# Optimization experiments

Measured on AMD Instinct MI355X. Metric: run time of the kernel, lower is better.

## Reference

```python
import jax, jax.numpy as jnp
import numpy as np

LOG2 = float(np.log(2.0))

def ssp(x):
    # shifted softplus, the PhysNet-family activation: softplus(x) - ln(2)
    return jax.nn.softplus(x) - LOG2

def setup_inputs() -> dict:
    key = jax.random.key(0)
    k1, k2, k3, k4, k5 = jax.random.split(key, 5)
    N, E, D_EDGE, D_RBF = 50000, 640000, 128, 64
    vi = jax.random.normal(k1, (N, D_EDGE), dtype=jnp.float32)
    rbf = jax.random.uniform(k2, (E, D_RBF), dtype=jnp.float32)
    edge_index = jax.random.randint(k3, (2, E), 0, N, dtype=jnp.int64)
    # torch.nn.Linear params: y = x @ W.T + b, W ~ U(-1/sqrt(fan_in), 1/sqrt(fan_in))
    s1 = 1.0 / np.sqrt(D_RBF)
    s2 = 1.0 / np.sqrt(3 * D_EDGE)
    W_rbf = jax.random.uniform(k4, (D_EDGE, D_RBF), jnp.float32, -s1, s1)
    b_rbf = jnp.zeros((D_EDGE,), jnp.float32)
    W_cat = jax.random.uniform(k5, (D_EDGE, 3 * D_EDGE), jnp.float32, -s2, s2)
    b_cat = jnp.zeros((D_EDGE,), jnp.float32)
    return {"vi": vi, "rbf": rbf, "W_rbf": W_rbf, "b_rbf": b_rbf,
            "W_cat": W_cat, "b_cat": b_cat, "edge_index": edge_index}

def reference(vi, rbf, W_rbf, b_rbf, W_cat, b_cat, edge_index):
    # gather endpoint features per edge: [E, D]
    h_i = vi[edge_index[0], :]
    h_j = vi[edge_index[1], :]
    rbf_proj = rbf @ W_rbf.T + b_rbf              # [E, D]
    concat_msg = jnp.concatenate([rbf_proj, h_j, h_i], axis=-1)  # [E, 3D]
    m_ji = ssp(concat_msg @ W_cat.T + b_cat)      # [E, D]
    return m_ji
```

## Files before the change

kernel.cpp:

```cpp
#include <hip/hip_runtime.h>
#include <cmath>

#define D  128
#define DR 64

typedef float fx4    __attribute__((ext_vector_type(4)));
typedef float f32x16 __attribute__((ext_vector_type(16)));
typedef short short8v __attribute__((ext_vector_type(8)));

__device__ __forceinline__ float ssp_f(float x) {
  float m = fmaxf(x, 0.0f);
  float t = __expf(-fabsf(x));
  return m + __logf(1.0f + t) - 0.69314718055994531f;
}

__device__ __forceinline__ short f2bf(float f) {
  unsigned u = __float_as_uint(f);
  u = (u + 0x7FFFu + ((u >> 16) & 1u)) >> 16;
  return (short)u;
}

__device__ __forceinline__ float bf2f(unsigned short h) {
  return __uint_as_float(((unsigned)h) << 16);
}

__device__ __forceinline__ short8v cvt8(const float* p) {
  fx4 lo = *(const fx4*)p;
  fx4 hi = *(const fx4*)(p + 4);
  short8v r;
  r[0] = f2bf(lo.x); r[1] = f2bf(lo.y); r[2] = f2bf(lo.z); r[3] = f2bf(lo.w);
  r[4] = f2bf(hi.x); r[5] = f2bf(hi.y); r[6] = f2bf(hi.z); r[7] = f2bf(hi.w);
  return r;
}

__global__ __launch_bounds__(256) void prep_kernel(
    const float* __restrict__ vi, const float* __restrict__ W_cat,
    const float* __restrict__ W_rbf, const float* __restrict__ b_rbf,
    const float* __restrict__ b_cat,
    unsigned short* __restrict__ PjH, unsigned short* __restrict__ PiH,
    float* __restrict__ weff, unsigned short* __restrict__ weffh,
    float* __restrict__ beff, int N, int nbt, int write_bf16)
{
  const int t = threadIdx.x;
  if ((int)blockIdx.x >= nbt) {
    int gid = ((int)blockIdx.x - nbt) * 256 + t;
    if (gid < D * DR) {
      int o = gid >> 6;
      int r = gid & 63;
      float acc = 0.0f;
      #pragma unroll 8
      for (int d = 0; d < D; ++d)
        acc = fmaf(W_cat[o * 384 + d], W_rbf[d * DR + r], acc);
      weff[gid] = acc;
      if (write_bf16) weffh[gid] = (unsigned short)f2bf(acc);
    }
    if (gid < D) {
      float acc = b_cat[gid];
      #pragma unroll 8
      for (int d = 0; d < D; ++d)
        acc = fmaf(b_rbf[d], W_cat[gid * 384 + d], acc);
      beff[gid] = acc;
    }
    return;
  }

  const int lane = t & 63;
  const int col  = lane & 31;
  const int half = lane >> 5;
  const long wid  = (long)blockIdx.x * 4 + (t >> 6);
  const long base = wid * 64;
  if (base >= (long)N) return;

  #pragma unroll
  for (int tile = 0; tile < 2; ++tile) {
    const long tb = base + (long)tile * 32;
    if (tb >= (long)N) break;
    long nr = tb + col; if (nr > (long)N - 1) nr = (long)N - 1;

    const float* arow = vi + nr * D + half * 8;
    short8v A[8];
    #pragma unroll
    for (int ks = 0; ks < 8; ++ks)
      A[ks] = cvt8(&arow[ks * 16]);

    #pragma unroll
    for (int ct = 0; ct < 8; ++ct) {
      const int off = 128 + (ct >> 2) * 128;
      const int o   = (ct & 3) * 32 + col;
      const float* wrow = W_cat + (long)o * 384 + off + half * 8;

      f32x16 acc = (f32x16)(0.0f);
      #pragma unroll
      for (int ks = 0; ks < 8; ++ks) {
        short8v Bv = cvt8(&wrow[ks * 16]);
        acc = __builtin_amdgcn_mfma_f32_32x32x16_bf16(A[ks], Bv, acc, 0, 0, 0);
      }

      unsigned short* P = (ct < 4) ? PjH : PiH;
      const int cb = (ct & 3) * 32;
      #pragma unroll
      for (int reg = 0; reg < 16; ++reg) {
        const int erl = (reg & 3) + 8 * (reg >> 2) + 4 * half;
        const long nn = tb + erl;
        if (nn < (long)N)
          P[nn * D + cb + col] = (unsigned short)f2bf(acc[reg]);
      }
    }
  }
}

__global__ __launch_bounds__(64) void edge_mfma_kernel(
    const float* __restrict__ rbf, const int* __restrict__ eidx,
    const unsigned short* __restrict__ weffh, const float* __restrict__ beff,
    const unsigned short* __restrict__ PjH, const unsigned short* __restrict__ PiH,
    float* __restrict__ out, int E)
{
  const int lane = threadIdx.x & 63;
  const int row  = lane & 31;
  const int half = lane >> 5;
  const long base = (long)blockIdx.x * 64;
  if (base >= (long)E) return;

  short8v B[4][4];
  #pragma unroll
  for (int ct = 0; ct < 4; ++ct) {
    #pragma unroll
    for (int ks = 0; ks < 4; ++ks)
      B[ct][ks] = *(const short8v*)&weffh[(ct * 32 + row) * DR + ks * 16 + half * 8];
  }
  float bias[4];
  #pragma unroll
  for (int ct = 0; ct < 4; ++ct) bias[ct] = beff[ct * 32 + row];

  #pragma unroll
  for (int tile = 0; tile < 2; ++tile) {
    const long tb = base + (long)tile * 32;
    if (tb >= (long)E) break;
    long er = tb + row; if (er > (long)E - 1) er = (long)E - 1;

    const float* arow = rbf + er * DR + half * 8;
    short8v A[4];
    #pragma unroll
    for (int ks = 0; ks < 4; ++ks) {
      fx4 lo = __builtin_nontemporal_load((const fx4*)&arow[ks * 16]);
      fx4 hi = __builtin_nontemporal_load((const fx4*)&arow[ks * 16 + 4]);
      short8v a;
      a[0] = f2bf(lo.x); a[1] = f2bf(lo.y); a[2] = f2bf(lo.z); a[3] = f2bf(lo.w);
      a[4] = f2bf(hi.x); a[5] = f2bf(hi.y); a[6] = f2bf(hi.z); a[7] = f2bf(hi.w);
      A[ks] = a;
    }

    const int iv = eidx[er];
    const int jv = eidx[(long)E + er];

    #pragma unroll
    for (int ct = 0; ct < 4; ++ct) {
      float gj[16], gi[16];
      #pragma unroll
      for (int reg = 0; reg < 16; ++reg) {
        const int erl = (reg & 3) + 8 * (reg >> 2) + 4 * half;
        const int j = __shfl(jv, erl);
        const int i = __shfl(iv, erl);
        gj[reg] = bf2f(PjH[(long)j * D + ct * 32 + row]);
        gi[reg] = bf2f(PiH[(long)i * D + ct * 32 + row]);
      }
      __builtin_amdgcn_sched_barrier(0);

      f32x16 acc = (f32x16)(0.0f);
      acc = __builtin_amdgcn_mfma_f32_32x32x16_bf16(A[0], B[ct][0], acc, 0, 0, 0);
      acc = __builtin_amdgcn_mfma_f32_32x32x16_bf16(A[1], B[ct][1], acc, 0, 0, 0);
      acc = __builtin_amdgcn_mfma_f32_32x32x16_bf16(A[2], B[ct][2], acc, 0, 0, 0);
      acc = __builtin_amdgcn_mfma_f32_32x32x16_bf16(A[3], B[ct][3], acc, 0, 0, 0);

      #pragma unroll
      for (int reg = 0; reg < 16; ++reg) {
        const int erl = (reg & 3) + 8 * (reg >> 2) + 4 * half;
        const long ge = tb + erl;
        const float v = ssp_f(acc[reg] + gj[reg] + gi[reg] + bias[ct]);
        if (ge < (long)E)
          __builtin_nontemporal_store(v, &out[ge * D + ct * 32 + row]);
      }
    }
  }
}

template<int K, int WS, int WOFF, bool GATHER, bool INIT, bool FINAL>
__global__ __launch_bounds__(256) void pass_kernel(
    const float* __restrict__ src, const int* __restrict__ gidx,
    const float* __restrict__ W, const float* __restrict__ beff,
    float* __restrict__ out, int E)
{
  int e = blockIdx.x * 256 + threadIdx.x;
  if (e >= E) return;
  long rowi = GATHER ? (long)gidx[e] : (long)e;

  float4 rv[K / 4];
  const float4* sp = (const float4*)(src + rowi * K);
  #pragma unroll
  for (int c = 0; c < K / 4; ++c) rv[c] = sp[c];

  float* orow = out + (long)e * D;
  for (int ob = 0; ob < D; ob += 4) {
    float acc[4];
    if (INIT) {
      float4 b4 = *(const float4*)&beff[ob];
      acc[0] = b4.x; acc[1] = b4.y; acc[2] = b4.z; acc[3] = b4.w;
    } else {
      float4 p4 = *(const float4*)&orow[ob];
      acc[0] = p4.x; acc[1] = p4.y; acc[2] = p4.z; acc[3] = p4.w;
    }
    #pragma unroll
    for (int k = 0; k < 4; ++k) {
      const float4* wv = (const float4*)&W[(long)(ob + k) * WS + WOFF];
      float a = acc[k];
      #pragma unroll
      for (int c = 0; c < K / 4; ++c) {
        float4 w4 = wv[c]; float4 r4 = rv[c];
        a = fmaf(w4.x, r4.x, a); a = fmaf(w4.y, r4.y, a);
        a = fmaf(w4.z, r4.z, a); a = fmaf(w4.w, r4.w, a);
      }
      acc[k] = a;
    }
    float4 o4;
    o4.x = FINAL ? ssp_f(acc[0]) : acc[0];
    o4.y = FINAL ? ssp_f(acc[1]) : acc[1];
    o4.z = FINAL ? ssp_f(acc[2]) : acc[2];
    o4.w = FINAL ? ssp_f(acc[3]) : acc[3];
    *(float4*)&orow[ob] = o4;
  }
}

extern "C" void kernel_launch(void* const* d_in, const int* in_sizes, int n_in,
                              void* d_out, int out_size, void* d_ws, size_t ws_size,
                              hipStream_t stream)
{
  const float* vi    = (const float*)d_in[0];
  const float* rbf   = (const float*)d_in[1];
  const float* W_rbf = (const float*)d_in[2];
  const float* b_rbf = (const float*)d_in[3];
  const float* W_cat = (const float*)d_in[4];
  const float* b_cat = (const float*)d_in[5];
  const int*   eidx  = (const int*)d_in[6];

  const int N = in_sizes[0] / D;
  const int E = in_sizes[6] / 2;
  float* out = (float*)d_out;

  float* ws   = (float*)d_ws;
  float* weff = ws;
  float* beff = ws + D * DR;
  unsigned short* weffh = (unsigned short*)(ws + 8448);
  unsigned short* PjH = (unsigned short*)(ws + 8448 + 4096);
  unsigned short* PiH = PjH + (size_t)N * D;
  size_t need = (8448 + 4096 + (size_t)N * 128) * sizeof(float);

  const int use_fast = (ws_size >= need && E >= 1);

  if (use_fast) {
    long twaves = ((long)N + 63) / 64;
    int nbt = (int)((twaves + 3) / 4);
    prep_kernel<<<nbt + 32, 256, 0, stream>>>(vi, W_cat, W_rbf, b_rbf, b_cat,
                                              PjH, PiH, weff, weffh, beff,
                                              N, nbt, 1);
    int fblocks = (int)(((long)E + 63) / 64);
    edge_mfma_kernel<<<fblocks, 64, 0, stream>>>(rbf, eidx, weffh, beff,
                                                 PjH, PiH, out, E);
  } else {
    prep_kernel<<<32, 256, 0, stream>>>(vi, W_cat, W_rbf, b_rbf, b_cat,
                                        PjH, PiH, weff, weffh, beff,
                                        N, 0, 0);
    int eblocks = (E + 255) / 256;
    pass_kernel<DR, DR, 0,  false, true,  false><<<eblocks, 256, 0, stream>>>(rbf, nullptr,  weff,  beff, out, E);
    pass_kernel<D, 384, 128, true, false, false><<<eblocks, 256, 0, stream>>>(vi,  eidx + E, W_cat, beff, out, E);
    pass_kernel<D, 384, 256, true, false, true ><<<eblocks, 256, 0, stream>>>(vi,  eidx,     W_cat, beff, out, E);
  }
}
```

Before: 245.9 us.

## Restructure edge kernel to 16x16 MFMA tiles with double-buffered gathers

The edge kernel now handles 16 edges per 64-lane block using 16x16x32 bf16 MFMA instead of 64 edges with 32x32x16, which quadruples the block count. Gathers of the projected endpoint features are double-buffered across column tiles so that loads for the next tile are issued before the current tile's compute. Byte offsets are precomputed once per edge, and the bias is folded into the accumulator initialisation. B weights are reloaded per column tile rather than held in registers, which adds some global or cache traffic per block.

```diff
diff --git a/kernel.cpp b/kernel.cpp
--- a/kernel.cpp
+++ b/kernel.cpp
@@ -116,72 +116,78 @@
     float* __restrict__ out, int E)
 {
   const int lane = threadIdx.x & 63;
-  const int row  = lane & 31;
-  const int half = lane >> 5;
-  const long base = (long)blockIdx.x * 64;
-  if (base >= (long)E) return;
-
-  short8v B[4][4];
-  #pragma unroll
-  for (int ct = 0; ct < 4; ++ct) {
-    #pragma unroll
-    for (int ks = 0; ks < 4; ++ks)
-      B[ct][ks] = *(const short8v*)&weffh[(ct * 32 + row) * DR + ks * 16 + half * 8];
-  }
-  float bias[4];
-  #pragma unroll
-  for (int ct = 0; ct < 4; ++ct) bias[ct] = beff[ct * 32 + row];
-
-  #pragma unroll
-  for (int tile = 0; tile < 2; ++tile) {
-    const long tb = base + (long)tile * 32;
-    if (tb >= (long)E) break;
-    long er = tb + row; if (er > (long)E - 1) er = (long)E - 1;
-
-    const float* arow = rbf + er * DR + half * 8;
-    short8v A[4];
-    #pragma unroll
-    for (int ks = 0; ks < 4; ++ks) {
-      fx4 lo = __builtin_nontemporal_load((const fx4*)&arow[ks * 16]);
-      fx4 hi = __builtin_nontemporal_load((const fx4*)&arow[ks * 16 + 4]);
-      short8v a;
-      a[0] = f2bf(lo.x); a[1] = f2bf(lo.y); a[2] = f2bf(lo.z); a[3] = f2bf(lo.w);
-      a[4] = f2bf(hi.x); a[5] = f2bf(hi.y); a[6] = f2bf(hi.z); a[7] = f2bf(hi.w);
-      A[ks] = a;
-    }
-
-    const int iv = eidx[er];
-    const int jv = eidx[(long)E + er];
-
-    #pragma unroll
-    for (int ct = 0; ct < 4; ++ct) {
-      float gj[16], gi[16];
-      #pragma unroll
-      for (int reg = 0; reg < 16; ++reg) {
-        const int erl = (reg & 3) + 8 * (reg >> 2) + 4 * half;
-        const int j = __shfl(jv, erl);
-        const int i = __shfl(iv, erl);
-        gj[reg] = bf2f(PjH[(long)j * D + ct * 32 + row]);
-        gi[reg] = bf2f(PiH[(long)i * D + ct * 32 + row]);
-      }
-      __builtin_amdgcn_sched_barrier(0);
-
-      f32x16 acc = (f32x16)(0.0f);
-      acc = __builtin_amdgcn_mfma_f32_32x32x16_bf16(A[0], B[ct][0], acc, 0, 0, 0);
-      acc = __builtin_amdgcn_mfma_f32_32x32x16_bf16(A[1], B[ct][1], acc, 0, 0, 0);
-      acc = __builtin_amdgcn_mfma_f32_32x32x16_bf16(A[2], B[ct][2], acc, 0, 0, 0);
-      acc = __builtin_amdgcn_mfma_f32_32x32x16_bf16(A[3], B[ct][3], acc, 0, 0, 0);
-
-      #pragma unroll
-      for (int reg = 0; reg < 16; ++reg) {
-        const int erl = (reg & 3) + 8 * (reg >> 2) + 4 * half;
-        const long ge = tb + erl;
-        const float v = ssp_f(acc[reg] + gj[reg] + gi[reg] + bias[ct]);
-        if (ge < (long)E)
-          __builtin_nontemporal_store(v, &out[ge * D + ct * 32 + row]);
-      }
-    }
-  }
+  const int n16  = lane & 15;
+  const int kg   = lane >> 4;
+  const long tb  = (long)blockIdx.x * 16;
+  if (tb >= (long)E) return;
+
+  long ar = tb + n16; if (ar > (long)E - 1) ar = (long)E - 1;
+  const float* arow = rbf + ar * DR + kg * 8;
+  short8v A0, A1;
+  {
+    fx4 l0 = __builtin_nontemporal_load((const fx4*)&arow[0]);
+    fx4 h0 = __builtin_nontemporal_load((const fx4*)&arow[4]);
+    fx4 l1 = __builtin_nontemporal_load((const fx4*)&arow[32]);
+    fx4 h1 = __builtin_nontemporal_load((const fx4*)&arow[36]);
+    A0[0] = f2bf(l0.x); A0[1] = f2bf(l0.y); A0[2] = f2bf(l0.z); A0[3] = f2bf(l0.w);
+    A0[4] = f2bf(h0.x); A0[5] = f2bf(h0.y); A0[6] = f2bf(h0.z); A0[7] = f2bf(h0.w);
+    A1[0] = f2bf(l1.x); A1[1] = f2bf(l1.y); A1[2] = f2bf(l1.z); A1[3] = f2bf(l1.w);
+    A1[4] = f2bf(h1.x); A1[5] = f2bf(h1.y); A1[6] = f2bf(h1.z); A1[7] = f2bf(h1.w);
+  }
+
+  int joff[4], ioff[4], soff[4];
+  bool ok[4];
+  #pragma unroll
+  for (int reg = 0; reg < 4; ++reg) {
+    const long ge = tb + kg * 4 + reg;
+    ok[reg] = ge < (long)E;
+    const long gc = ok[reg] ? ge : (long)E - 1;
+    joff[reg] = eidx[(long)E + gc] * 256 + n16 * 2;
+    ioff[reg] = eidx[gc] * 256 + n16 * 2;
+    soff[reg] = (int)(ge * 512) + n16 * 4;
+  }
+
+  const char* PjB = (const char*)PjH;
+  const char* PiB = (const char*)PiH;
+  char* outB = (char*)out;
+
+#define ISSUE_G(gjv, giv, ct)                                                  \
+  { _Pragma("unroll")                                                          \
+    for (int reg = 0; reg < 4; ++reg) {                                        \
+      gjv[reg] = *(const unsigned short*)(PjB + (long)joff[reg] + (ct) * 32);  \
+      giv[reg] = *(const unsigned short*)(PiB + (long)ioff[reg] + (ct) * 32);  \
+    } }
+
+#define COMPUTE(ct, gjv, giv)                                                  \
+  { short8v B0 = *(const short8v*)&weffh[((ct) * 16 + n16) * DR + kg * 8];     \
+    short8v B1 = *(const short8v*)&weffh[((ct) * 16 + n16) * DR + 32 + kg * 8];\
+    const float bias = beff[(ct) * 16 + n16];                                  \
+    fx4 acc = {bias, bias, bias, bias};                                        \
+    acc = __builtin_amdgcn_mfma_f32_16x16x32_bf16(A0, B0, acc, 0, 0, 0);       \
+    acc = __builtin_amdgcn_mfma_f32_16x16x32_bf16(A1, B1, acc, 0, 0, 0);       \
+    _Pragma("unroll")                                                          \
+    for (int reg = 0; reg < 4; ++reg) {                                        \
+      const float v = ssp_f(acc[reg] + bf2f(gjv[reg]) + bf2f(giv[reg]));       \
+      if (ok[reg])                                                             \
+        __builtin_nontemporal_store(v, (float*)(outB + (long)soff[reg] + (ct) * 64)); \
+    } }
+
+  unsigned short gjA[4], giA[4], gjB[4], giB[4];
+
+  ISSUE_G(gjA, giA, 0);
+  #pragma unroll
+  for (int c2 = 0; c2 < 4; ++c2) {
+    const int ct0 = 2 * c2, ct1 = 2 * c2 + 1;
+    ISSUE_G(gjB, giB, ct1);
+    __builtin_amdgcn_sched_barrier(0);
+    COMPUTE(ct0, gjA, giA);
+    if (ct0 + 2 < 8) { ISSUE_G(gjA, giA, ct0 + 2); }
+    __builtin_amdgcn_sched_barrier(0);
+    COMPUTE(ct1, gjB, giB);
+  }
+
+#undef ISSUE_G
+#undef COMPUTE
 }
 
 template<int K, int WS, int WOFF, bool GATHER, bool INIT, bool FINAL>
@@ -262,7 +268,7 @@
     prep_kernel<<<nbt + 32, 256, 0, stream>>>(vi, W_cat, W_rbf, b_rbf, b_cat,
                                               PjH, PiH, weff, weffh, beff,
                                               N, nbt, 1);
-    int fblocks = (int)(((long)E + 63) / 64);
+    int fblocks = (int)(((long)E + 15) / 16);
     edge_mfma_kernel<<<fblocks, 64, 0, stream>>>(rbf, eidx, weffh, beff,
                                                  PjH, PiH, out, E);
   } else {
```

New measurement: 281.9 us. 14.6% more time.
